# Performance work log

Hardware: AMD Instinct MI355X
Metric: run time of the kernel (lower is better)

The kernel has to match this reference:

```python
import jax, jax.numpy as jnp
import numpy as np

N = 10000       # n_nodes
E = 640000      # n_edges (avg degree 64)
D_IN = 128      # in_feats
D_H = 128       # n_hidden
N_CLS = 64      # n_classes


def setup_inputs() -> dict:
    key = jax.random.key(0)
    k1, k2, k3, k4, k5, k6 = jax.random.split(key, 6)
    features = jax.random.normal(k1, (N, D_IN), dtype=jnp.float32)
    src = jax.random.randint(k2, (E,), 0, N, dtype=jnp.int32)
    dst = jax.random.randint(k3, (E,), 0, N, dtype=jnp.int32)
    s = 0.05  # small init scale to keep activations bounded across 3 layers
    # Stored as [in, out]; equivalent to torch Linear weight [out, in] transposed.
    W0 = jax.random.normal(k4, (D_IN, D_H), dtype=jnp.float32) * s
    W1 = jax.random.normal(k5, (D_H, D_H), dtype=jnp.float32) * s
    W2 = jax.random.normal(k6, (D_H, N_CLS), dtype=jnp.float32) * s
    return {"features": features, "W0": W0, "W1": W1, "W2": W2,
            "src": src, "dst": dst}


def reference(features, W0, W1, W2, src, dst):
    # GINConv with aggregator 'sum', eps=0 (learn_eps=False):
    #   h' = Linear(h + sum_{(u->v) in E} h[u] scattered to v)
    # Dropout is identity at inference; 'activation' is unused in the module.
    def gin_layer(h, W):
        agg = jax.ops.segment_sum(h[src], dst, num_segments=N)  # [N, d]
        return (h + agg) @ W

    h = gin_layer(features, W0)
    h = gin_layer(h, W1)
    h = gin_layer(h, W2)
    return h
```

## Files before the change

### kernel.cpp

```cpp
#include <hip/hip_runtime.h>
#include <hip/hip_bf16.h>

#define NN 10000
#define NE 640000
#define D_IN 128
#define D_H 128
#define N_CLS 64
#define CAP 160
#define GRP 157
#define CAPC 4800
#define CCS 16
#define SENT 10000
#define EPB 1024
#define AB 625
#define CB 1251
#define WB 80

__device__ __forceinline__ float blo(unsigned u) { return __uint_as_float(u << 16); }
__device__ __forceinline__ float bhi(unsigned u) { return __uint_as_float(u & 0xffff0000u); }
__device__ __forceinline__ unsigned short f2bf(float f) {
    unsigned u = __float_as_uint(f);
    return (unsigned short)((u + 0x7fffu + ((u >> 16) & 1u)) >> 16);
}
__device__ __forceinline__ unsigned packbf(float a, float b) {
    return (unsigned)f2bf(a) | ((unsigned)f2bf(b) << 16);
}

__global__ __launch_bounds__(256) void prep_a(const int* __restrict__ src,
                                              const int* __restrict__ dst,
                                              int* __restrict__ coarse_cnt,
                                              unsigned* __restrict__ coarse,
                                              const float* __restrict__ feat,
                                              unsigned* __restrict__ hb0,
                                              const float* __restrict__ W0,
                                              const float* __restrict__ W1,
                                              const float* __restrict__ W2,
                                              unsigned* __restrict__ wb0,
                                              unsigned* __restrict__ wb1,
                                              unsigned* __restrict__ wb2) {
    int bid = blockIdx.x;
    if (bid >= AB + CB) {
        int t = (bid - AB - CB) * 256 + threadIdx.x;
        if (t < 8192) {
            int kp = t >> 7, j = t & 127;
            wb0[t] = packbf(W0[(2 * kp) * 128 + j], W0[(2 * kp + 1) * 128 + j]);
        } else if (t < 16384) {
            int tt = t - 8192, kp = tt >> 7, j = tt & 127;
            wb1[tt] = packbf(W1[(2 * kp) * 128 + j], W1[(2 * kp + 1) * 128 + j]);
        } else if (t < 20480) {
            int tt = t - 16384, kp = tt >> 6, j = tt & 63;
            wb2[tt] = packbf(W2[(2 * kp) * 64 + j], W2[(2 * kp + 1) * 64 + j]);
        }
        return;
    }
    if (bid >= AB) {
        int t = (bid - AB) * 256 + threadIdx.x;
        if (t < NN * 32) {
            float4 f = ((const float4*)feat)[t];
            ((uint2*)hb0)[t] = make_uint2(packbf(f.x, f.y), packbf(f.z, f.w));
        } else if (t < (NN + 1) * 32) {
            ((uint2*)hb0)[t] = make_uint2(0u, 0u);
        }
        return;
    }
    __shared__ unsigned stage[EPB];
    __shared__ int hist[GRP], gbase[GRP], cur[GRP];
    const int t = threadIdx.x;
    for (int i = t; i < GRP; i += 256) hist[i] = 0;
    __syncthreads();
    const int e0 = bid * EPB;
    for (int i = t; i < EPB; i += 256) {
        int s = src[e0 + i];
        int d = dst[e0 + i];
        stage[i] = (unsigned)s | ((unsigned)d << 16);
        atomicAdd(&hist[d >> 6], 1);
    }
    __syncthreads();
    for (int i = t; i < GRP; i += 256) {
        gbase[i] = atomicAdd(&coarse_cnt[i * CCS], hist[i]);
        cur[i] = 0;
    }
    __syncthreads();
    for (int i = t; i < EPB; i += 256) {
        unsigned u = stage[i];
        int g = u >> 22;
        int r = atomicAdd(&cur[g], 1);
        coarse[g * CAPC + gbase[g] + r] = u;
    }
}

__global__ __launch_bounds__(1024) void prep_b(const int* __restrict__ coarse_cnt,
                                               const unsigned* __restrict__ coarse,
                                               int* __restrict__ cnt,
                                               unsigned short* __restrict__ colbuf) {
    __shared__ int cur[64];
    __shared__ unsigned short sbuf[64][CAP];
    const int g = blockIdx.x;
    const int t = threadIdx.x;
    if (t < 64) cur[t] = 0;
    __syncthreads();
    const int m = coarse_cnt[g * CCS];
    const unsigned* cb = coarse + g * CAPC;
    for (int i = t; i < m; i += 1024) {
        unsigned u = cb[i];
        int s = (int)(u & 0xFFFFu);
        int dl = (int)(u >> 16) - (g << 6);
        int r = atomicAdd(&cur[dl], 1);
        sbuf[dl][r] = (unsigned short)s;
    }
    __syncthreads();
    if (t < 64) {
        int n = (g << 6) + t;
        if (n < NN) {
            int c = cur[t];
            int pad = (32 - (c & 31)) & 31;
            for (int k = 0; k < pad; ++k) sbuf[t][c + k] = (unsigned short)SENT;
            cnt[n] = c + pad;
        }
    }
    __syncthreads();
    const uint4* s4 = (const uint4*)sbuf;
    for (int idx = t; idx < 64 * (CAP / 8); idx += 1024) {
        int node = (g << 6) + (idx / (CAP / 8));
        if (node < NN)
            ((uint4*)colbuf)[(size_t)node * (CAP / 8) + (idx % (CAP / 8))] = s4[idx];
    }
}

template <int J, bool LAST>
__global__ __launch_bounds__(256, 4) void gin_layer(const uint4* __restrict__ hb4,
                                                    const int* __restrict__ cnt,
                                                    const unsigned short* __restrict__ colbuf,
                                                    const unsigned* __restrict__ Wb,
                                                    unsigned short* __restrict__ outb,
                                                    float* __restrict__ outf) {
    constexpr int M = 4;
    __shared__ float xs[M][D_H];
    const int base = blockIdx.x * M;
    const int tid = threadIdx.x;
    const int wave = tid >> 6;
    const int lane = tid & 63;
    const int sub = lane >> 4;
    const int off = lane & 15;

    const int n = __builtin_amdgcn_readfirstlane(base + wave);
    float a0, a1, a2, a3, a4, a5, a6, a7;
    if (sub == 0) {
        uint4 u = hb4[n * 16 + off];
        a0 = blo(u.x); a1 = bhi(u.x); a2 = blo(u.y); a3 = bhi(u.y);
        a4 = blo(u.z); a5 = bhi(u.z); a6 = blo(u.w); a7 = bhi(u.w);
    } else {
        a0 = a1 = a2 = a3 = a4 = a5 = a6 = a7 = 0.f;
    }
    const int NCH = __builtin_amdgcn_readfirstlane(cnt[n]) >> 5;
    const uint2* cl = (const uint2*)(colbuf + n * CAP);
    const int sh = (sub & 1) << 4;
    uint2 p0 = cl[0], p1 = cl[1], p2 = cl[2], p3 = cl[3];
    uint2 p4 = cl[4], p5 = cl[5], p6 = cl[6], p7 = cl[7];
    for (int c = 0; c < NCH; ++c) {
        unsigned w0 = (sub & 2) ? p0.y : p0.x;
        unsigned w1 = (sub & 2) ? p1.y : p1.x;
        unsigned w2 = (sub & 2) ? p2.y : p2.x;
        unsigned w3 = (sub & 2) ? p3.y : p3.x;
        unsigned w4 = (sub & 2) ? p4.y : p4.x;
        unsigned w5 = (sub & 2) ? p5.y : p5.x;
        unsigned w6 = (sub & 2) ? p6.y : p6.x;
        unsigned w7 = (sub & 2) ? p7.y : p7.x;
        int s0 = (int)((w0 >> sh) & 0xffffu);
        int s1 = (int)((w1 >> sh) & 0xffffu);
        int s2 = (int)((w2 >> sh) & 0xffffu);
        int s3 = (int)((w3 >> sh) & 0xffffu);
        int s4 = (int)((w4 >> sh) & 0xffffu);
        int s5 = (int)((w5 >> sh) & 0xffffu);
        int s6 = (int)((w6 >> sh) & 0xffffu);
        int s7 = (int)((w7 >> sh) & 0xffffu);
        uint4 u0 = hb4[s0 * 16 + off];
        uint4 u1 = hb4[s1 * 16 + off];
        uint4 u2 = hb4[s2 * 16 + off];
        uint4 u3 = hb4[s3 * 16 + off];
        uint4 u4 = hb4[s4 * 16 + off];
        uint4 u5 = hb4[s5 * 16 + off];
        uint4 u6 = hb4[s6 * 16 + off];
        uint4 u7 = hb4[s7 * 16 + off];
        {
            const uint2* nx = cl + 8 * (c + 1);
            p0 = nx[0]; p1 = nx[1]; p2 = nx[2]; p3 = nx[3];
            p4 = nx[4]; p5 = nx[5]; p6 = nx[6]; p7 = nx[7];
        }
        a0 += ((blo(u0.x) + blo(u1.x)) + (blo(u2.x) + blo(u3.x)))
            + ((blo(u4.x) + blo(u5.x)) + (blo(u6.x) + blo(u7.x)));
        a1 += ((bhi(u0.x) + bhi(u1.x)) + (bhi(u2.x) + bhi(u3.x)))
            + ((bhi(u4.x) + bhi(u5.x)) + (bhi(u6.x) + bhi(u7.x)));
        a2 += ((blo(u0.y) + blo(u1.y)) + (blo(u2.y) + blo(u3.y)))
            + ((blo(u4.y) + blo(u5.y)) + (blo(u6.y) + blo(u7.y)));
        a3 += ((bhi(u0.y) + bhi(u1.y)) + (bhi(u2.y) + bhi(u3.y)))
            + ((bhi(u4.y) + bhi(u5.y)) + (bhi(u6.y) + bhi(u7.y)));
        a4 += ((blo(u0.z) + blo(u1.z)) + (blo(u2.z) + blo(u3.z)))
            + ((blo(u4.z) + blo(u5.z)) + (blo(u6.z) + blo(u7.z)));
        a5 += ((bhi(u0.z) + bhi(u1.z)) + (bhi(u2.z) + bhi(u3.z)))
            + ((bhi(u4.z) + bhi(u5.z)) + (bhi(u6.z) + bhi(u7.z)));
        a6 += ((blo(u0.w) + blo(u1.w)) + (blo(u2.w) + blo(u3.w)))
            + ((blo(u4.w) + blo(u5.w)) + (blo(u6.w) + blo(u7.w)));
        a7 += ((bhi(u0.w) + bhi(u1.w)) + (bhi(u2.w) + bhi(u3.w)))
            + ((bhi(u4.w) + bhi(u5.w)) + (bhi(u6.w) + bhi(u7.w)));
    }
    a0 += __shfl_xor(a0, 16); a0 += __shfl_xor(a0, 32);
    a1 += __shfl_xor(a1, 16); a1 += __shfl_xor(a1, 32);
    a2 += __shfl_xor(a2, 16); a2 += __shfl_xor(a2, 32);
    a3 += __shfl_xor(a3, 16); a3 += __shfl_xor(a3, 32);
    a4 += __shfl_xor(a4, 16); a4 += __shfl_xor(a4, 32);
    a5 += __shfl_xor(a5, 16); a5 += __shfl_xor(a5, 32);
    a6 += __shfl_xor(a6, 16); a6 += __shfl_xor(a6, 32);
    a7 += __shfl_xor(a7, 16); a7 += __shfl_xor(a7, 32);
    if (sub == 0) {
        *(float4*)&xs[wave][8 * off]     = make_float4(a0, a1, a2, a3);
        *(float4*)&xs[wave][8 * off + 4] = make_float4(a4, a5, a6, a7);
    }
    __syncthreads();

    constexpr int G = 256 / J;
    constexpr int NM = M / G;
    const int gq = tid / J;
    const int j = tid % J;
    const int mbase = gq * NM;
    float acc[NM];
#pragma unroll
    for (int m = 0; m < NM; ++m) acc[m] = 0.f;
    for (int k = 0; k < D_H; k += 4) {
        unsigned wp0 = Wb[(k >> 1) * J + j];
        unsigned wp1 = Wb[((k >> 1) + 1) * J + j];
        float w0 = blo(wp0), w1 = bhi(wp0), w2 = blo(wp1), w3 = bhi(wp1);
#pragma unroll
        for (int m = 0; m < NM; ++m) {
            float4 xv = *(const float4*)&xs[mbase + m][k];
            acc[m] += xv.x * w0 + xv.y * w1 + xv.z * w2 + xv.w * w3;
        }
    }
#pragma unroll
    for (int m = 0; m < NM; ++m) {
        int n2 = base + mbase + m;
        if (LAST) __builtin_nontemporal_store(acc[m], &outf[(size_t)n2 * J + j]);
        else      __builtin_nontemporal_store(f2bf(acc[m]), &outb[(size_t)n2 * J + j]);
    }
    if (!LAST && blockIdx.x == 0 && tid < 32) {
        ((uint2*)(outb + (size_t)SENT * D_H))[tid] = make_uint2(0u, 0u);
    }
}

extern "C" void kernel_launch(void* const* d_in, const int* in_sizes, int n_in,
                              void* d_out, int out_size, void* d_ws, size_t ws_size,
                              hipStream_t stream) {
    const float* feat = (const float*)d_in[0];
    const float* W0   = (const float*)d_in[1];
    const float* W1   = (const float*)d_in[2];
    const float* W2   = (const float*)d_in[3];
    const int*   src  = (const int*)d_in[4];
    const int*   dst  = (const int*)d_in[5];
    float* out = (float*)d_out;

    int* coarse_cnt        = (int*)d_ws;
    int* cnt               = coarse_cnt + GRP * CCS;
    unsigned short* colbuf = (unsigned short*)(cnt + NN + 8);
    unsigned* coarse       = (unsigned*)(colbuf + (size_t)NN * CAP);
    unsigned* hb0          = coarse + (size_t)GRP * CAPC;
    unsigned* hb1          = hb0 + (size_t)(NN + 1) * 64;
    unsigned* hb2          = hb1 + (size_t)(NN + 1) * 64;
    unsigned* wb0          = hb2 + (size_t)(NN + 1) * 64;
    unsigned* wb1          = wb0 + 8192;
    unsigned* wb2          = wb1 + 8192;

    hipMemsetAsync(coarse_cnt, 0, GRP * CCS * sizeof(int), stream);
    prep_a<<<AB + CB + WB, 256, 0, stream>>>(src, dst, coarse_cnt, coarse, feat, hb0,
                                             W0, W1, W2, wb0, wb1, wb2);
    prep_b<<<GRP, 1024, 0, stream>>>(coarse_cnt, coarse, cnt, colbuf);

    gin_layer<D_H, false><<<NN / 4, 256, 0, stream>>>((const uint4*)hb0, cnt, colbuf, wb0,
                                                      (unsigned short*)hb1, nullptr);
    gin_layer<D_H, false><<<NN / 4, 256, 0, stream>>>((const uint4*)hb1, cnt, colbuf, wb1,
                                                      (unsigned short*)hb2, nullptr);
    gin_layer<N_CLS, true><<<NN / 4, 256, 0, stream>>>((const uint4*)hb2, cnt, colbuf, wb2,
                                                       nullptr, out);
}
```

Before: 147.2 us.

## Reorder last GIN layer: project to 64 classes before aggregating

Uses linearity, (h+A h)W2 = hW2 + A(hW2), to fuse the W2 projection into the second layer's kernel and aggregate a 64-wide bf16 tensor in the final layer instead of a 128-wide one. This halves the gather traffic of the third aggregation and removes one dense matmul pass over aggregated data. It also drops the nontemporal stores on the intermediate outputs. The cost is an extra bf16 rounding of the projected values before aggregation, plus more LDS and work in the middle kernel.

```diff
diff --git a/kernel.cpp b/kernel.cpp
--- a/kernel.cpp
+++ b/kernel.cpp
@@ -127,13 +127,11 @@
     }
 }
 
-template <int J, bool LAST>
-__global__ __launch_bounds__(256, 4) void gin_layer(const uint4* __restrict__ hb4,
-                                                    const int* __restrict__ cnt,
-                                                    const unsigned short* __restrict__ colbuf,
-                                                    const unsigned* __restrict__ Wb,
-                                                    unsigned short* __restrict__ outb,
-                                                    float* __restrict__ outf) {
+__global__ __launch_bounds__(256, 4) void gin_layer1(const uint4* __restrict__ hb4,
+                                                     const int* __restrict__ cnt,
+                                                     const unsigned short* __restrict__ colbuf,
+                                                     const unsigned* __restrict__ Wb,
+                                                     unsigned short* __restrict__ outb) {
     constexpr int M = 4;
     __shared__ float xs[M][D_H];
     const int base = blockIdx.x * M;
@@ -218,6 +216,7 @@
     }
     __syncthreads();
 
+    constexpr int J = D_H;
     constexpr int G = 256 / J;
     constexpr int NM = M / G;
     const int gq = tid / J;
@@ -239,11 +238,215 @@
 #pragma unroll
     for (int m = 0; m < NM; ++m) {
         int n2 = base + mbase + m;
-        if (LAST) __builtin_nontemporal_store(acc[m], &outf[(size_t)n2 * J + j]);
-        else      __builtin_nontemporal_store(f2bf(acc[m]), &outb[(size_t)n2 * J + j]);
-    }
-    if (!LAST && blockIdx.x == 0 && tid < 32) {
+        outb[(size_t)n2 * J + j] = f2bf(acc[m]);
+    }
+    if (blockIdx.x == 0 && tid < 32) {
         ((uint2*)(outb + (size_t)SENT * D_H))[tid] = make_uint2(0u, 0u);
+    }
+}
+
+__global__ __launch_bounds__(256, 4) void gin_mid(const uint4* __restrict__ hb4,
+                                                  const int* __restrict__ cnt,
+                                                  const unsigned short* __restrict__ colbuf,
+                                                  const unsigned* __restrict__ Wb1,
+                                                  const unsigned* __restrict__ Wb2,
+                                                  unsigned short* __restrict__ tb) {
+    constexpr int M = 4;
+    __shared__ float xs[M][D_H];
+    __shared__ float ys[M][136];
+    const int base = blockIdx.x * M;
+    const int tid = threadIdx.x;
+    const int wave = tid >> 6;
+    const int lane = tid & 63;
+    const int sub = lane >> 4;
+    const int off = lane & 15;
+
+    const int n = __builtin_amdgcn_readfirstlane(base + wave);
+    float a0, a1, a2, a3, a4, a5, a6, a7;
+    if (sub == 0) {
+        uint4 u = hb4[n * 16 + off];
+        a0 = blo(u.x); a1 = bhi(u.x); a2 = blo(u.y); a3 = bhi(u.y);
+        a4 = blo(u.z); a5 = bhi(u.z); a6 = blo(u.w); a7 = bhi(u.w);
+    } else {
+        a0 = a1 = a2 = a3 = a4 = a5 = a6 = a7 = 0.f;
+    }
+    const int NCH = __builtin_amdgcn_readfirstlane(cnt[n]) >> 5;
+    const uint2* cl = (const uint2*)(colbuf + n * CAP);
+    const int sh = (sub & 1) << 4;
+    uint2 p0 = cl[0], p1 = cl[1], p2 = cl[2], p3 = cl[3];
+    uint2 p4 = cl[4], p5 = cl[5], p6 = cl[6], p7 = cl[7];
+    for (int c = 0; c < NCH; ++c) {
+        unsigned w0 = (sub & 2) ? p0.y : p0.x;
+        unsigned w1 = (sub & 2) ? p1.y : p1.x;
+        unsigned w2 = (sub & 2) ? p2.y : p2.x;
+        unsigned w3 = (sub & 2) ? p3.y : p3.x;
+        unsigned w4 = (sub & 2) ? p4.y : p4.x;
+        unsigned w5 = (sub & 2) ? p5.y : p5.x;
+        unsigned w6 = (sub & 2) ? p6.y : p6.x;
+        unsigned w7 = (sub & 2) ? p7.y : p7.x;
+        int s0 = (int)((w0 >> sh) & 0xffffu);
+        int s1 = (int)((w1 >> sh) & 0xffffu);
+        int s2 = (int)((w2 >> sh) & 0xffffu);
+        int s3 = (int)((w3 >> sh) & 0xffffu);
+        int s4 = (int)((w4 >> sh) & 0xffffu);
+        int s5 = (int)((w5 >> sh) & 0xffffu);
+        int s6 = (int)((w6 >> sh) & 0xffffu);
+        int s7 = (int)((w7 >> sh) & 0xffffu);
+        uint4 u0 = hb4[s0 * 16 + off];
+        uint4 u1 = hb4[s1 * 16 + off];
+        uint4 u2 = hb4[s2 * 16 + off];
+        uint4 u3 = hb4[s3 * 16 + off];
+        uint4 u4 = hb4[s4 * 16 + off];
+        uint4 u5 = hb4[s5 * 16 + off];
+        uint4 u6 = hb4[s6 * 16 + off];
+        uint4 u7 = hb4[s7 * 16 + off];
+        {
+            const uint2* nx = cl + 8 * (c + 1);
+            p0 = nx[0]; p1 = nx[1]; p2 = nx[2]; p3 = nx[3];
+            p4 = nx[4]; p5 = nx[5]; p6 = nx[6]; p7 = nx[7];
+        }
+        a0 += ((blo(u0.x) + blo(u1.x)) + (blo(u2.x) + blo(u3.x)))
+            + ((blo(u4.x) + blo(u5.x)) + (blo(u6.x) + blo(u7.x)));
+        a1 += ((bhi(u0.x) + bhi(u1.x)) + (bhi(u2.x) + bhi(u3.x)))
+            + ((bhi(u4.x) + bhi(u5.x)) + (bhi(u6.x) + bhi(u7.x)));
+        a2 += ((blo(u0.y) + blo(u1.y)) + (blo(u2.y) + blo(u3.y)))
+            + ((blo(u4.y) + blo(u5.y)) + (blo(u6.y) + blo(u7.y)));
+        a3 += ((bhi(u0.y) + bhi(u1.y)) + (bhi(u2.y) + bhi(u3.y)))
+            + ((bhi(u4.y) + bhi(u5.y)) + (bhi(u6.y) + bhi(u7.y)));
+        a4 += ((blo(u0.z) + blo(u1.z)) + (blo(u2.z) + blo(u3.z)))
+            + ((blo(u4.z) + blo(u5.z)) + (blo(u6.z) + blo(u7.z)));
+        a5 += ((bhi(u0.z) + bhi(u1.z)) + (bhi(u2.z) + bhi(u3.z)))
+            + ((bhi(u4.z) + bhi(u5.z)) + (bhi(u6.z) + bhi(u7.z)));
+        a6 += ((blo(u0.w) + blo(u1.w)) + (blo(u2.w) + blo(u3.w)))
+            + ((blo(u4.w) + blo(u5.w)) + (blo(u6.w) + blo(u7.w)));
+        a7 += ((bhi(u0.w) + bhi(u1.w)) + (bhi(u2.w) + bhi(u3.w)))
+            + ((bhi(u4.w) + bhi(u5.w)) + (bhi(u6.w) + bhi(u7.w)));
+    }
+    a0 += __shfl_xor(a0, 16); a0 += __shfl_xor(a0, 32);
+    a1 += __shfl_xor(a1, 16); a1 += __shfl_xor(a1, 32);
+    a2 += __shfl_xor(a2, 16); a2 += __shfl_xor(a2, 32);
+    a3 += __shfl_xor(a3, 16); a3 += __shfl_xor(a3, 32);
+    a4 += __shfl_xor(a4, 16); a4 += __shfl_xor(a4, 32);
+    a5 += __shfl_xor(a5, 16); a5 += __shfl_xor(a5, 32);
+    a6 += __shfl_xor(a6, 16); a6 += __shfl_xor(a6, 32);
+    a7 += __shfl_xor(a7, 16); a7 += __shfl_xor(a7, 32);
+    if (sub == 0) {
+        *(float4*)&xs[wave][8 * off]     = make_float4(a0, a1, a2, a3);
+        *(float4*)&xs[wave][8 * off + 4] = make_float4(a4, a5, a6, a7);
+    }
+    __syncthreads();
+
+    {
+        constexpr int J = D_H;
+        constexpr int G = 256 / J;
+        constexpr int NM = M / G;
+        const int gq = tid / J;
+        const int j = tid % J;
+        const int mbase = gq * NM;
+        float acc[NM];
+#pragma unroll
+        for (int m = 0; m < NM; ++m) acc[m] = 0.f;
+        for (int k = 0; k < D_H; k += 4) {
+            unsigned wp0 = Wb1[(k >> 1) * J + j];
+            unsigned wp1 = Wb1[((k >> 1) + 1) * J + j];
+            float w0 = blo(wp0), w1 = bhi(wp0), w2 = blo(wp1), w3 = bhi(wp1);
+#pragma unroll
+            for (int m = 0; m < NM; ++m) {
+                float4 xv = *(const float4*)&xs[mbase + m][k];
+                acc[m] += xv.x * w0 + xv.y * w1 + xv.z * w2 + xv.w * w3;
+            }
+        }
+#pragma unroll
+        for (int m = 0; m < NM; ++m) ys[mbase + m][j] = acc[m];
+    }
+    __syncthreads();
+
+    {
+        constexpr int J = N_CLS;
+        const int j = tid & 63;
+        const int gm = tid >> 6;
+        float acc = 0.f;
+        for (int k = 0; k < D_H; k += 4) {
+            unsigned wp0 = Wb2[(k >> 1) * J + j];
+            unsigned wp1 = Wb2[((k >> 1) + 1) * J + j];
+            float w0 = blo(wp0), w1 = bhi(wp0), w2 = blo(wp1), w3 = bhi(wp1);
+            float4 xv = *(const float4*)&ys[gm][k];
+            acc += xv.x * w0 + xv.y * w1 + xv.z * w2 + xv.w * w3;
+        }
+        tb[(size_t)(base + gm) * J + j] = f2bf(acc);
+    }
+    if (blockIdx.x == 0 && tid < 16) {
+        ((uint2*)(tb + (size_t)SENT * N_CLS))[tid] = make_uint2(0u, 0u);
+    }
+}
+
+__global__ __launch_bounds__(256, 4) void agg3(const uint4* __restrict__ tb4,
+                                               const int* __restrict__ cnt,
+                                               const unsigned short* __restrict__ colbuf,
+                                               float* __restrict__ outf) {
+    constexpr int M = 4;
+    const int base = blockIdx.x * M;
+    const int tid = threadIdx.x;
+    const int wave = tid >> 6;
+    const int lane = tid & 63;
+    const int sub = lane >> 3;
+    const int off = lane & 7;
+
+    const int n = __builtin_amdgcn_readfirstlane(base + wave);
+    float a0, a1, a2, a3, a4, a5, a6, a7;
+    if (sub == 0) {
+        uint4 u = tb4[n * 8 + off];
+        a0 = blo(u.x); a1 = bhi(u.x); a2 = blo(u.y); a3 = bhi(u.y);
+        a4 = blo(u.z); a5 = bhi(u.z); a6 = blo(u.w); a7 = bhi(u.w);
+    } else {
+        a0 = a1 = a2 = a3 = a4 = a5 = a6 = a7 = 0.f;
+    }
+    const int NCH = __builtin_amdgcn_readfirstlane(cnt[n]) >> 5;
+    const uint2* cl = (const uint2*)(colbuf + n * CAP);
+    const int hi4 = sub >> 2;
+    const int wsel = (sub >> 1) & 1;
+    const int sh = (sub & 1) << 4;
+    uint2 p0 = cl[0], p1 = cl[1], p2 = cl[2], p3 = cl[3];
+    uint2 p4 = cl[4], p5 = cl[5], p6 = cl[6], p7 = cl[7];
+    for (int c = 0; c < NCH; ++c) {
+        unsigned q0 = hi4 ? (wsel ? p1.y : p1.x) : (wsel ? p0.y : p0.x);
+        unsigned q1 = hi4 ? (wsel ? p3.y : p3.x) : (wsel ? p2.y : p2.x);
+        unsigned q2 = hi4 ? (wsel ? p5.y : p5.x) : (wsel ? p4.y : p4.x);
+        unsigned q3 = hi4 ? (wsel ? p7.y : p7.x) : (wsel ? p6.y : p6.x);
+        int s0 = (int)((q0 >> sh) & 0xffffu);
+        int s1 = (int)((q1 >> sh) & 0xffffu);
+        int s2 = (int)((q2 >> sh) & 0xffffu);
+        int s3 = (int)((q3 >> sh) & 0xffffu);
+        uint4 u0 = tb4[s0 * 8 + off];
+        uint4 u1 = tb4[s1 * 8 + off];
+        uint4 u2 = tb4[s2 * 8 + off];
+        uint4 u3 = tb4[s3 * 8 + off];
+        {
+            const uint2* nx = cl + 8 * (c + 1);
+            p0 = nx[0]; p1 = nx[1]; p2 = nx[2]; p3 = nx[3];
+            p4 = nx[4]; p5 = nx[5]; p6 = nx[6]; p7 = nx[7];
+        }
+        a0 += (blo(u0.x) + blo(u1.x)) + (blo(u2.x) + blo(u3.x));
+        a1 += (bhi(u0.x) + bhi(u1.x)) + (bhi(u2.x) + bhi(u3.x));
+        a2 += (blo(u0.y) + blo(u1.y)) + (blo(u2.y) + blo(u3.y));
+        a3 += (bhi(u0.y) + bhi(u1.y)) + (bhi(u2.y) + bhi(u3.y));
+        a4 += (blo(u0.z) + blo(u1.z)) + (blo(u2.z) + blo(u3.z));
+        a5 += (bhi(u0.z) + bhi(u1.z)) + (bhi(u2.z) + bhi(u3.z));
+        a6 += (blo(u0.w) + blo(u1.w)) + (blo(u2.w) + blo(u3.w));
+        a7 += (bhi(u0.w) + bhi(u1.w)) + (bhi(u2.w) + bhi(u3.w));
+    }
+    a0 += __shfl_xor(a0, 8); a0 += __shfl_xor(a0, 16); a0 += __shfl_xor(a0, 32);
+    a1 += __shfl_xor(a1, 8); a1 += __shfl_xor(a1, 16); a1 += __shfl_xor(a1, 32);
+    a2 += __shfl_xor(a2, 8); a2 += __shfl_xor(a2, 16); a2 += __shfl_xor(a2, 32);
+    a3 += __shfl_xor(a3, 8); a3 += __shfl_xor(a3, 16); a3 += __shfl_xor(a3, 32);
+    a4 += __shfl_xor(a4, 8); a4 += __shfl_xor(a4, 16); a4 += __shfl_xor(a4, 32);
+    a5 += __shfl_xor(a5, 8); a5 += __shfl_xor(a5, 16); a5 += __shfl_xor(a5, 32);
+    a6 += __shfl_xor(a6, 8); a6 += __shfl_xor(a6, 16); a6 += __shfl_xor(a6, 32);
+    a7 += __shfl_xor(a7, 8); a7 += __shfl_xor(a7, 16); a7 += __shfl_xor(a7, 32);
+    if (sub == 0) {
+        float* o = outf + (size_t)n * N_CLS + 8 * off;
+        *(float4*)o       = make_float4(a0, a1, a2, a3);
+        *(float4*)(o + 4) = make_float4(a4, a5, a6, a7);
     }
 }
 
@@ -268,16 +471,15 @@
     unsigned* wb0          = hb2 + (size_t)(NN + 1) * 64;
     unsigned* wb1          = wb0 + 8192;
     unsigned* wb2          = wb1 + 8192;
+    unsigned short* tb     = (unsigned short*)hb2;
 
     hipMemsetAsync(coarse_cnt, 0, GRP * CCS * sizeof(int), stream);
     prep_a<<<AB + CB + WB, 256, 0, stream>>>(src, dst, coarse_cnt, coarse, feat, hb0,
                                              W0, W1, W2, wb0, wb1, wb2);
     prep_b<<<GRP, 1024, 0, stream>>>(coarse_cnt, coarse, cnt, colbuf);
 
-    gin_layer<D_H, false><<<NN / 4, 256, 0, stream>>>((const uint4*)hb0, cnt, colbuf, wb0,
-                                                      (unsigned short*)hb1, nullptr);
-    gin_layer<D_H, false><<<NN / 4, 256, 0, stream>>>((const uint4*)hb1, cnt, colbuf, wb1,
-                                                      (unsigned short*)hb2, nullptr);
-    gin_layer<N_CLS, true><<<NN / 4, 256, 0, stream>>>((const uint4*)hb2, cnt, colbuf, wb2,
-                                                       nullptr, out);
-}
+    gin_layer1<<<NN / 4, 256, 0, stream>>>((const uint4*)hb0, cnt, colbuf, wb0,
+                                           (unsigned short*)hb1);
+    gin_mid<<<NN / 4, 256, 0, stream>>>((const uint4*)hb1, cnt, colbuf, wb1, wb2, tb);
+    agg3<<<NN / 4, 256, 0, stream>>>((const uint4*)tb, cnt, colbuf, out);
+}
```

New measurement: 142.9 us. 2.9% less time.
